# Kernel optimization log

Measured on AMD Instinct MI355X. Metric: run time of the kernel, lower is better.

Reference implementation:

```python
import jax, jax.numpy as jnp
import numpy as np


def _gcs_conv(x, a, w1, w2, b):
    # GCSConv: relu(A @ x W1 + x W2 + b);  x:[B,N,F], a:[B,N,N]
    return jax.nn.relu(jnp.einsum('bij,bjh->bih', a, x @ w1) + x @ w2 + b)


def _topk_pool(x, a, p, ratio=0.5):
    # score y = x . p/||p||, keep top ceil(ratio*N) nodes per graph,
    # gate kept node features with sigmoid(y), slice adjacency rows+cols.
    y = x @ (p / jnp.linalg.norm(p))            # [B, N]
    k = int(np.ceil(ratio * y.shape[1]))
    yk, idx = jax.lax.top_k(y, k)               # [B, k]
    xk = jnp.take_along_axis(x, idx[:, :, None], axis=1)
    xk = xk * jax.nn.sigmoid(yk)[:, :, None]    # gated node features [B,k,H]
    ak = jnp.take_along_axis(a, idx[:, :, None], axis=1)
    ak = jnp.take_along_axis(ak, idx[:, None, :], axis=2)  # [B,k,k]
    return xk, ak


def setup_inputs() -> dict:
    B, N, F0, H, C = 256, 512, 128, 32, 16
    key = jax.random.key(0)
    ks = jax.random.split(key, 12)
    s = lambda fan: 1.0 / np.sqrt(fan)
    return {
        'x': jax.random.normal(ks[0], (B, N, F0), jnp.float32),
        'a': jax.random.uniform(ks[1], (B, N, N), jnp.float32),
        'w1_1': jax.random.normal(ks[2], (F0, H), jnp.float32) * s(F0),
        'w2_1': jax.random.normal(ks[3], (F0, H), jnp.float32) * s(F0),
        'b1': jnp.zeros((H,), jnp.float32),
        'w1_2': jax.random.normal(ks[4], (H, H), jnp.float32) * s(H),
        'w2_2': jax.random.normal(ks[5], (H, H), jnp.float32) * s(H),
        'b2': jnp.zeros((H,), jnp.float32),
        'w1_3': jax.random.normal(ks[6], (H, H), jnp.float32) * s(H),
        'w2_3': jax.random.normal(ks[7], (H, H), jnp.float32) * s(H),
        'b3': jnp.zeros((H,), jnp.float32),
        'p_pool': jax.random.normal(ks[8], (H,), jnp.float32),
        'wd': jax.random.normal(ks[9], (H, C), jnp.float32) * s(H),
        'bd': jnp.zeros((C,), jnp.float32),
    }


def reference(x, a, w1_1, w2_1, b1, w1_2, w2_2, b2, w1_3, w2_3, b3, p_pool, wd, bd):
    x = _gcs_conv(x, a, w1_1, w2_1, b1)
    # NOTE: original code reuses pool1 twice -> shared p_pool for both stages
    x1, a1 = _topk_pool(x, a, p_pool)
    x1 = _gcs_conv(x1, a1, w1_2, w2_2, b2)
    x2, a2 = _topk_pool(x1, a1, p_pool)
    x2 = _gcs_conv(x2, a2, w1_3, w2_3, b3)
    pooled = jnp.mean(x2, axis=1)               # GlobalAvgPool over nodes [B,H]
    return jax.nn.softmax(pooled @ wd + bd, axis=-1)
```

## Files before the change

kernel.cpp:

```cpp
#include <hip/hip_runtime.h>
#include <cmath>

#define B 256
#define N0 512
#define F0 128
#define H 32
#define NC 16

typedef short v8s __attribute__((ext_vector_type(8)));
typedef float v4f __attribute__((ext_vector_type(4)));

__device__ inline ushort bf16_rne(float f) {
  unsigned u = __float_as_uint(f);
  unsigned r = (u + 0x7FFF + ((u >> 16) & 1)) >> 16;
  return (ushort)r;
}
__device__ inline float bf16_f(ushort s) { return __uint_as_float((unsigned)s << 16); }

template<int F, int RPT>
__global__ __launch_bounds__(256) void k_xw(
    const float* __restrict__ x, const float* __restrict__ w1,
    const float* __restrict__ w2, const float* __restrict__ bias,
    float* __restrict__ h, float* __restrict__ g) {
  __shared__ float w1t[H][F + 4];
  __shared__ float w2t[H][F + 4];
  __shared__ float bs[H];
  const int tid = threadIdx.x;
  for (int i = tid; i < F * H; i += 256) {
    int f = i >> 5, hc = i & 31;
    w1t[hc][f] = w1[i];
    w2t[hc][f] = w2[i];
  }
  if (tid < H) bs[tid] = bias[tid];
  __syncthreads();
  const int hq = tid & 7;
  const int rq = tid >> 3;
  const size_t row0 = (size_t)blockIdx.x * (32 * RPT) + (size_t)rq * RPT;
  const float* xb = x + row0 * F;
  float acc1[RPT][4];
  float acc2[RPT][4];
  #pragma unroll
  for (int r = 0; r < RPT; ++r)
    for (int c = 0; c < 4; ++c) { acc1[r][c] = 0.f; acc2[r][c] = 0.f; }
  for (int f0 = 0; f0 < F; f0 += 4) {
    float4 w1v[4], w2v[4];
    #pragma unroll
    for (int hh = 0; hh < 4; ++hh) {
      w1v[hh] = *(const float4*)&w1t[hq * 4 + hh][f0];
      w2v[hh] = *(const float4*)&w2t[hq * 4 + hh][f0];
    }
    #pragma unroll
    for (int r = 0; r < RPT; ++r) {
      float4 xv = *(const float4*)(xb + (size_t)r * F + f0);
      #pragma unroll
      for (int hh = 0; hh < 4; ++hh) {
        acc1[r][hh] += xv.x * w1v[hh].x + xv.y * w1v[hh].y + xv.z * w1v[hh].z + xv.w * w1v[hh].w;
        acc2[r][hh] += xv.x * w2v[hh].x + xv.y * w2v[hh].y + xv.z * w2v[hh].z + xv.w * w2v[hh].w;
      }
    }
  }
  #pragma unroll
  for (int r = 0; r < RPT; ++r) {
    size_t o = (row0 + r) * H + hq * 4;
    float4 hv = make_float4(acc1[r][0], acc1[r][1], acc1[r][2], acc1[r][3]);
    float4 gv = make_float4(acc2[r][0] + bs[hq * 4 + 0], acc2[r][1] + bs[hq * 4 + 1],
                            acc2[r][2] + bs[hq * 4 + 2], acc2[r][3] + bs[hq * 4 + 3]);
    *(float4*)(h + o) = hv;
    *(float4*)(g + o) = gv;
  }
}

__global__ __launch_bounds__(256) void k_trans_d(
    const float* __restrict__ hsrc, ushort* __restrict__ hTh, ushort* __restrict__ hTl) {
  __shared__ ushort thi[H][72];
  __shared__ ushort tlo[H][72];
  const int tid = threadIdx.x;
  const int b = blockIdx.x;
  const int jr = tid >> 2, kq = tid & 3;
  const int hh = tid >> 3, seg = tid & 7;
  for (int j0 = 0; j0 < N0; j0 += 64) {
    if (j0) __syncthreads();
    const float* src = hsrc + (((size_t)b * N0) + j0 + jr) * H + kq * 8;
    float4 v0 = *(const float4*)src;
    float4 v1 = *(const float4*)(src + 4);
    float vv[8] = {v0.x, v0.y, v0.z, v0.w, v1.x, v1.y, v1.z, v1.w};
    #pragma unroll
    for (int i = 0; i < 8; ++i) {
      ushort hi = bf16_rne(vv[i]);
      thi[kq * 8 + i][jr] = hi;
      tlo[kq * 8 + i][jr] = bf16_rne(vv[i] - bf16_f(hi));
    }
    __syncthreads();
    size_t o = ((size_t)b * H + hh) * N0 + j0 + seg * 8;
    *(uint4*)&hTh[o] = *(const uint4*)&thi[hh][seg * 8];
    *(uint4*)&hTl[o] = *(const uint4*)&tlo[hh][seg * 8];
  }
}

template<int K>
__global__ __launch_bounds__(256) void k_trans_s(
    const float* __restrict__ hd, const int* __restrict__ idx,
    ushort* __restrict__ hTh, ushort* __restrict__ hTl) {
  const int tid = threadIdx.x;
  const int b = blockIdx.x;
  for (int t = tid; t < K * 4; t += 256) {
    int row = t >> 2, kq = t & 3;
    int gid = idx[(size_t)b * K + row];
    const float* src = hd + (((size_t)b * K) + row) * H + kq * 8;
    float4 v0 = *(const float4*)src;
    float4 v1 = *(const float4*)(src + 4);
    float vv[8] = {v0.x, v0.y, v0.z, v0.w, v1.x, v1.y, v1.z, v1.w};
    #pragma unroll
    for (int i = 0; i < 8; ++i) {
      ushort hi = bf16_rne(vv[i]);
      size_t o = ((size_t)b * H + kq * 8 + i) * N0 + gid;
      hTh[o] = hi;
      hTl[o] = bf16_rne(vv[i] - bf16_f(hi));
    }
  }
}

template<int NROW>
__global__ __launch_bounds__(256) void k_ammx(
    const float* __restrict__ a0, const int* __restrict__ rid,
    const ushort* __restrict__ hTh, const ushort* __restrict__ hTl,
    const float* __restrict__ g, float* __restrict__ out) {
  constexpr int RB = 64;
  constexpr int KC = 32;
  constexpr int ASP = KC + 8;
  __shared__ ushort ah[RB][ASP];
  __shared__ ushort al[RB][ASP];
  __shared__ ushort bh[H][ASP];
  __shared__ ushort bl[H][ASP];
  __shared__ int rowid[RB];
  const int tid = threadIdx.x;
  const int b = blockIdx.x;
  const int row0 = blockIdx.y * RB;
  if (tid < RB) rowid[tid] = rid ? rid[(size_t)b * NROW + row0 + tid] : row0 + tid;
  __syncthreads();
  const int wave = tid >> 6, lane = tid & 63;
  const int m = lane & 15, quad = lane >> 4;
  const int sr = tid >> 2, skq = tid & 3;
  const int shh = tid >> 3, sseg = tid & 7;
  const float* abase = a0 + (size_t)b * N0 * N0;
  const ushort* bhsrc = hTh + ((size_t)b * H + shh) * N0 + sseg * 4;
  const ushort* blsrc = hTl + ((size_t)b * H + shh) * N0 + sseg * 4;
  v4f acc0 = {0.f, 0.f, 0.f, 0.f};
  v4f acc1 = {0.f, 0.f, 0.f, 0.f};
  for (int k0 = 0; k0 < N0; k0 += KC) {
    if (k0) __syncthreads();
    {
      const float* ap = abase + (size_t)rowid[sr] * N0 + k0 + skq * 4;
      float4 v0 = *(const float4*)ap;
      float4 v1 = *(const float4*)(ap + 16);
      ushort4 h0, l0, h1, l1;
      h0.x = bf16_rne(v0.x); l0.x = bf16_rne(v0.x - bf16_f(h0.x));
      h0.y = bf16_rne(v0.y); l0.y = bf16_rne(v0.y - bf16_f(h0.y));
      h0.z = bf16_rne(v0.z); l0.z = bf16_rne(v0.z - bf16_f(h0.z));
      h0.w = bf16_rne(v0.w); l0.w = bf16_rne(v0.w - bf16_f(h0.w));
      h1.x = bf16_rne(v1.x); l1.x = bf16_rne(v1.x - bf16_f(h1.x));
      h1.y = bf16_rne(v1.y); l1.y = bf16_rne(v1.y - bf16_f(h1.y));
      h1.z = bf16_rne(v1.z); l1.z = bf16_rne(v1.z - bf16_f(h1.z));
      h1.w = bf16_rne(v1.w); l1.w = bf16_rne(v1.w - bf16_f(h1.w));
      *(ushort4*)&ah[sr][skq * 4] = h0;      *(ushort4*)&al[sr][skq * 4] = l0;
      *(ushort4*)&ah[sr][skq * 4 + 16] = h1; *(ushort4*)&al[sr][skq * 4 + 16] = l1;
    }
    {
      *(ushort4*)&bh[shh][sseg * 4] = *(const ushort4*)(bhsrc + k0);
      *(ushort4*)&bl[shh][sseg * 4] = *(const ushort4*)(blsrc + k0);
    }
    __syncthreads();
    const int arow = wave * 16 + m;
    v8s Ah = *(const v8s*)&ah[arow][quad * 8];
    v8s Al = *(const v8s*)&al[arow][quad * 8];
    v8s Bh0 = *(const v8s*)&bh[m][quad * 8];
    v8s Bh1 = *(const v8s*)&bh[16 + m][quad * 8];
    v8s Bl0 = *(const v8s*)&bl[m][quad * 8];
    v8s Bl1 = *(const v8s*)&bl[16 + m][quad * 8];
    acc0 = __builtin_amdgcn_mfma_f32_16x16x32_bf16(Ah, Bh0, acc0, 0, 0, 0);
    acc1 = __builtin_amdgcn_mfma_f32_16x16x32_bf16(Ah, Bh1, acc1, 0, 0, 0);
    acc0 = __builtin_amdgcn_mfma_f32_16x16x32_bf16(Al, Bh0, acc0, 0, 0, 0);
    acc1 = __builtin_amdgcn_mfma_f32_16x16x32_bf16(Al, Bh1, acc1, 0, 0, 0);
    acc0 = __builtin_amdgcn_mfma_f32_16x16x32_bf16(Ah, Bl0, acc0, 0, 0, 0);
    acc1 = __builtin_amdgcn_mfma_f32_16x16x32_bf16(Ah, Bl1, acc1, 0, 0, 0);
  }
  #pragma unroll
  for (int reg = 0; reg < 4; ++reg) {
    int row = row0 + wave * 16 + quad * 4 + reg;
    size_t o0 = ((size_t)b * NROW + row) * H + m;
    size_t o1 = o0 + 16;
    float v0 = acc0[reg] + g[o0];
    float v1 = acc1[reg] + g[o1];
    out[o0] = fmaxf(v0, 0.f);
    out[o1] = fmaxf(v1, 0.f);
  }
}

__global__ __launch_bounds__(256) void k_zero(float4* __restrict__ p, int n4) {
  int i = blockIdx.x * 256 + threadIdx.x;
  if (i < n4) p[i] = make_float4(0.f, 0.f, 0.f, 0.f);
}

template<int NN, int K>
__global__ __launch_bounds__(256) void k_topk(
    const float* __restrict__ x, const float* __restrict__ p,
    const int* __restrict__ prev_idx,
    float* __restrict__ xg, int* __restrict__ out_idx) {
  __shared__ float ys[NN];
  __shared__ int is[NN];
  __shared__ float ps[H];
  __shared__ float pns;
  const int tid = threadIdx.x;
  const int b = blockIdx.x;
  if (tid < H) ps[tid] = p[tid];
  __syncthreads();
  if (tid == 0) {
    float s = 0.f;
    for (int i = 0; i < H; ++i) s += ps[i] * ps[i];
    pns = 1.f / sqrtf(s);
  }
  __syncthreads();
  for (int i = tid; i < NN; i += 256) {
    const float* xr = x + ((size_t)b * NN + i) * H;
    float s = 0.f;
    #pragma unroll
    for (int f = 0; f < H; ++f) s += xr[f] * ps[f];
    ys[i] = s * pns;
    is[i] = i;
  }
  for (int k = 2; k <= NN; k <<= 1) {
    for (int j = k >> 1; j > 0; j >>= 1) {
      __syncthreads();
      for (int i = tid; i < NN; i += 256) {
        int ixj = i ^ j;
        if (ixj > i) {
          float v0 = ys[i], v1 = ys[ixj];
          int i0 = is[i], i1 = is[ixj];
          bool pre = (v1 > v0) || (v1 == v0 && i1 < i0);
          bool doswap = ((i & k) == 0) ? pre : !pre;
          if (doswap) { ys[i] = v1; ys[ixj] = v0; is[i] = i1; is[ixj] = i0; }
        }
      }
    }
  }
  for (int k = 2; k <= K; k <<= 1) {
    for (int j = k >> 1; j > 0; j >>= 1) {
      __syncthreads();
      for (int i = tid; i < K; i += 256) {
        int ixj = i ^ j;
        if (ixj > i && ixj < K) {
          float v0 = ys[i], v1 = ys[ixj];
          int i0 = is[i], i1 = is[ixj];
          bool pre = (i1 < i0);
          bool doswap = ((i & k) == 0) ? pre : !pre;
          if (doswap) { ys[i] = v1; ys[ixj] = v0; is[i] = i1; is[ixj] = i0; }
        }
      }
    }
  }
  __syncthreads();
  for (int t = tid; t < K * H; t += 256) {
    int kk = t >> 5, f = t & 31;
    int loc = is[kk];
    float gate = 1.f / (1.f + expf(-ys[kk]));
    xg[((size_t)b * K + kk) * H + f] = x[((size_t)b * NN + loc) * H + f] * gate;
  }
  for (int t = tid; t < K; t += 256)
    out_idx[(size_t)b * K + t] = prev_idx ? prev_idx[(size_t)b * NN + is[t]] : is[t];
}

__global__ __launch_bounds__(128) void k_head(
    const float* __restrict__ xl3, const float* __restrict__ wd,
    const float* __restrict__ bd, float* __restrict__ out) {
  __shared__ float part[4][H];
  __shared__ float pooled[H];
  __shared__ float wds[H * NC];
  __shared__ float logits[NC];
  const int tid = threadIdx.x;
  const int b = blockIdx.x;
  for (int i = tid; i < H * NC; i += 128) wds[i] = wd[i];
  const int f = tid & 31, nq = tid >> 5;
  float s = 0.f;
  for (int n = nq * 32; n < nq * 32 + 32; ++n)
    s += xl3[((size_t)b * 128 + n) * H + f];
  part[nq][f] = s;
  __syncthreads();
  if (tid < H)
    pooled[tid] = (part[0][tid] + part[1][tid] + part[2][tid] + part[3][tid]) * (1.f / 128.f);
  __syncthreads();
  if (tid < NC) {
    float acc = bd[tid];
    for (int i = 0; i < H; ++i) acc += pooled[i] * wds[i * NC + tid];
    logits[tid] = acc;
  }
  __syncthreads();
  if (tid == 0) {
    float mx = logits[0];
    for (int i = 1; i < NC; ++i) mx = fmaxf(mx, logits[i]);
    float e[NC], se = 0.f;
    for (int i = 0; i < NC; ++i) { e[i] = expf(logits[i] - mx); se += e[i]; }
    float inv = 1.f / se;
    for (int i = 0; i < NC; ++i) out[(size_t)b * NC + i] = e[i] * inv;
  }
}

extern "C" void kernel_launch(void* const* d_in, const int* in_sizes, int n_in,
                              void* d_out, int out_size, void* d_ws, size_t ws_size,
                              hipStream_t stream) {
  (void)in_sizes; (void)n_in; (void)out_size; (void)ws_size;
  const float* x    = (const float*)d_in[0];
  const float* a    = (const float*)d_in[1];
  const float* w1_1 = (const float*)d_in[2];
  const float* w2_1 = (const float*)d_in[3];
  const float* b1   = (const float*)d_in[4];
  const float* w1_2 = (const float*)d_in[5];
  const float* w2_2 = (const float*)d_in[6];
  const float* b2   = (const float*)d_in[7];
  const float* w1_3 = (const float*)d_in[8];
  const float* w2_3 = (const float*)d_in[9];
  const float* b3   = (const float*)d_in[10];
  const float* pp   = (const float*)d_in[11];
  const float* wd   = (const float*)d_in[12];
  const float* bd   = (const float*)d_in[13];
  float* out = (float*)d_out;

  char* w = (char*)d_ws;
  auto take = [&](size_t bytes) { char* r = w; w += (bytes + 255) & ~(size_t)255; return r; };
  float*  h1  = (float*) take((size_t)B * N0 * H * 4);
  float*  g1  = (float*) take((size_t)B * N0 * H * 4);
  ushort* hTh = (ushort*)take((size_t)B * H * N0 * 2);
  ushort* hTl = (ushort*)take((size_t)B * H * N0 * 2);
  float*  xl1 = (float*) take((size_t)B * N0 * H * 4);
  int*    id1 = (int*)   take((size_t)B * 256 * 4);
  float*  xg1 = (float*) take((size_t)B * 256 * H * 4);
  float*  h2  = (float*) take((size_t)B * 256 * H * 4);
  float*  g2  = (float*) take((size_t)B * 256 * H * 4);
  float*  xl2 = (float*) take((size_t)B * 256 * H * 4);
  int*    id2 = (int*)   take((size_t)B * 128 * 4);
  float*  xg2 = (float*) take((size_t)B * 128 * H * 4);
  float*  h3  = (float*) take((size_t)B * 128 * H * 4);
  float*  g3  = (float*) take((size_t)B * 128 * H * 4);
  float*  xl3 = (float*) take((size_t)B * 128 * H * 4);
  const int hT4 = (int)((size_t)B * H * N0 * 2 * 2 / 16);

  k_xw<F0, 2><<<dim3(B * N0 / 64), dim3(256), 0, stream>>>(x, w1_1, w2_1, b1, h1, g1);
  k_trans_d<<<dim3(B), dim3(256), 0, stream>>>(h1, hTh, hTl);
  k_ammx<512><<<dim3(B, 8), dim3(256), 0, stream>>>(a, nullptr, hTh, hTl, g1, xl1);
  k_topk<512, 256><<<dim3(B), dim3(256), 0, stream>>>(xl1, pp, nullptr, xg1, id1);
  k_xw<H, 4><<<dim3(B * 256 / 128), dim3(256), 0, stream>>>(xg1, w1_2, w2_2, b2, h2, g2);
  k_zero<<<dim3((hT4 + 255) / 256), dim3(256), 0, stream>>>((float4*)hTh, hT4);
  k_trans_s<256><<<dim3(B), dim3(256), 0, stream>>>(h2, id1, hTh, hTl);
  k_ammx<256><<<dim3(B, 4), dim3(256), 0, stream>>>(a, id1, hTh, hTl, g2, xl2);
  k_topk<256, 128><<<dim3(B), dim3(256), 0, stream>>>(xl2, pp, id1, xg2, id2);
  k_xw<H, 4><<<dim3(B * 128 / 128), dim3(256), 0, stream>>>(xg2, w1_3, w2_3, b3, h3, g3);
  k_zero<<<dim3((hT4 + 255) / 256), dim3(256), 0, stream>>>((float4*)hTh, hT4);
  k_trans_s<128><<<dim3(B), dim3(256), 0, stream>>>(h3, id2, hTh, hTl);
  k_ammx<128><<<dim3(B, 2), dim3(256), 0, stream>>>(a, id2, hTh, hTl, g3, xl3);
  k_head<<<dim3(B), dim3(128), 0, stream>>>(xl3, wd, bd, out);
}
```

Before: 601.6 us.

## Fuse transposes, pooling scores, and gated gathers into neighboring GCS kernels

The first XW kernel now writes the bf16 hi/lo transposed H directly, which removes the separate transpose pass and the fp32 h1 round trip. The A·H kernel computes the top-k score y in its epilogue through shuffle reductions, so top-k only sorts a precomputed score vector. The gather-and-gate step moves into the next XW kernel, using indices plus per-row gates, which relies on linearity to scale the outputs. Scatter transposes become an inverse-index dense write that also removes the separate zeroing kernels. The catch is the extra epilogue work in the A·H kernel and irregular gathered loads in XW.

```diff
diff --git a/kernel.cpp b/kernel.cpp
--- a/kernel.cpp
+++ b/kernel.cpp
@@ -9,6 +9,7 @@
 
 typedef short v8s __attribute__((ext_vector_type(8)));
 typedef float v4f __attribute__((ext_vector_type(4)));
+typedef unsigned short v8u __attribute__((ext_vector_type(8)));
 
 __device__ inline ushort bf16_rne(float f) {
   unsigned u = __float_as_uint(f);
@@ -18,13 +19,15 @@
 __device__ inline float bf16_f(ushort s) { return __uint_as_float((unsigned)s << 16); }
 
 template<int F, int RPT>
-__global__ __launch_bounds__(256) void k_xw(
+__global__ __launch_bounds__(256) void k_xw1(
     const float* __restrict__ x, const float* __restrict__ w1,
     const float* __restrict__ w2, const float* __restrict__ bias,
-    float* __restrict__ h, float* __restrict__ g) {
+    ushort* __restrict__ hTh, ushort* __restrict__ hTl, float* __restrict__ g) {
   __shared__ float w1t[H][F + 4];
   __shared__ float w2t[H][F + 4];
   __shared__ float bs[H];
+  __shared__ __align__(16) ushort thi[H][72];
+  __shared__ __align__(16) ushort tlo[H][72];
   const int tid = threadIdx.x;
   for (int i = tid; i < F * H; i += 256) {
     int f = i >> 5, hc = i & 31;
@@ -62,61 +65,121 @@
   #pragma unroll
   for (int r = 0; r < RPT; ++r) {
     size_t o = (row0 + r) * H + hq * 4;
-    float4 hv = make_float4(acc1[r][0], acc1[r][1], acc1[r][2], acc1[r][3]);
-    float4 gv = make_float4(acc2[r][0] + bs[hq * 4 + 0], acc2[r][1] + bs[hq * 4 + 1],
-                            acc2[r][2] + bs[hq * 4 + 2], acc2[r][3] + bs[hq * 4 + 3]);
-    *(float4*)(h + o) = hv;
-    *(float4*)(g + o) = gv;
-  }
-}
-
-__global__ __launch_bounds__(256) void k_trans_d(
-    const float* __restrict__ hsrc, ushort* __restrict__ hTh, ushort* __restrict__ hTl) {
-  __shared__ ushort thi[H][72];
-  __shared__ ushort tlo[H][72];
-  const int tid = threadIdx.x;
-  const int b = blockIdx.x;
-  const int jr = tid >> 2, kq = tid & 3;
-  const int hh = tid >> 3, seg = tid & 7;
-  for (int j0 = 0; j0 < N0; j0 += 64) {
-    if (j0) __syncthreads();
-    const float* src = hsrc + (((size_t)b * N0) + j0 + jr) * H + kq * 8;
-    float4 v0 = *(const float4*)src;
-    float4 v1 = *(const float4*)(src + 4);
-    float vv[8] = {v0.x, v0.y, v0.z, v0.w, v1.x, v1.y, v1.z, v1.w};
-    #pragma unroll
-    for (int i = 0; i < 8; ++i) {
-      ushort hi = bf16_rne(vv[i]);
-      thi[kq * 8 + i][jr] = hi;
-      tlo[kq * 8 + i][jr] = bf16_rne(vv[i] - bf16_f(hi));
-    }
-    __syncthreads();
-    size_t o = ((size_t)b * H + hh) * N0 + j0 + seg * 8;
-    *(uint4*)&hTh[o] = *(const uint4*)&thi[hh][seg * 8];
-    *(uint4*)&hTl[o] = *(const uint4*)&tlo[hh][seg * 8];
+    *(float4*)(g + o) = make_float4(acc2[r][0] + bs[hq * 4 + 0], acc2[r][1] + bs[hq * 4 + 1],
+                                    acc2[r][2] + bs[hq * 4 + 2], acc2[r][3] + bs[hq * 4 + 3]);
+    #pragma unroll
+    for (int c = 0; c < 4; ++c) {
+      float v = acc1[r][c];
+      ushort hi = bf16_rne(v);
+      thi[hq * 4 + c][rq * RPT + r] = hi;
+      tlo[hq * 4 + c][rq * RPT + r] = bf16_rne(v - bf16_f(hi));
+    }
+  }
+  __syncthreads();
+  const int b = blockIdx.x >> 3;
+  const int j0 = (blockIdx.x & 7) * 64;
+  const int hrow = tid >> 3, seg = tid & 7;
+  size_t o = ((size_t)b * H + hrow) * N0 + j0 + seg * 8;
+  *(uint4*)&hTh[o] = *(const uint4*)&thi[hrow][seg * 8];
+  *(uint4*)&hTl[o] = *(const uint4*)&tlo[hrow][seg * 8];
+}
+
+template<int NPREV, int K, int RPT>
+__global__ __launch_bounds__(256) void k_xwg(
+    const float* __restrict__ xsrc, const int* __restrict__ lidx,
+    const float* __restrict__ gate,
+    const float* __restrict__ w1, const float* __restrict__ w2,
+    const float* __restrict__ bias,
+    float* __restrict__ h, float* __restrict__ g) {
+  constexpr int F = H;
+  __shared__ float w1t[H][F + 4];
+  __shared__ float w2t[H][F + 4];
+  __shared__ float bs[H];
+  const int tid = threadIdx.x;
+  for (int i = tid; i < F * H; i += 256) {
+    int f = i >> 5, hc = i & 31;
+    w1t[hc][f] = w1[i];
+    w2t[hc][f] = w2[i];
+  }
+  if (tid < H) bs[tid] = bias[tid];
+  __syncthreads();
+  const int hq = tid & 7;
+  const int rq = tid >> 3;
+  const int row0 = blockIdx.x * (32 * RPT) + rq * RPT;
+  const int b = row0 / K;
+  const float* xg0 = xsrc + (size_t)b * NPREV * H;
+  int li[RPT];
+  float gt[RPT];
+  #pragma unroll
+  for (int r = 0; r < RPT; ++r) { li[r] = lidx[row0 + r]; gt[r] = gate[row0 + r]; }
+  float acc1[RPT][4];
+  float acc2[RPT][4];
+  #pragma unroll
+  for (int r = 0; r < RPT; ++r)
+    for (int c = 0; c < 4; ++c) { acc1[r][c] = 0.f; acc2[r][c] = 0.f; }
+  for (int f0 = 0; f0 < F; f0 += 4) {
+    float4 w1v[4], w2v[4];
+    #pragma unroll
+    for (int hh = 0; hh < 4; ++hh) {
+      w1v[hh] = *(const float4*)&w1t[hq * 4 + hh][f0];
+      w2v[hh] = *(const float4*)&w2t[hq * 4 + hh][f0];
+    }
+    #pragma unroll
+    for (int r = 0; r < RPT; ++r) {
+      float4 xv = *(const float4*)(xg0 + (size_t)li[r] * H + f0);
+      #pragma unroll
+      for (int hh = 0; hh < 4; ++hh) {
+        acc1[r][hh] += xv.x * w1v[hh].x + xv.y * w1v[hh].y + xv.z * w1v[hh].z + xv.w * w1v[hh].w;
+        acc2[r][hh] += xv.x * w2v[hh].x + xv.y * w2v[hh].y + xv.z * w2v[hh].z + xv.w * w2v[hh].w;
+      }
+    }
+  }
+  #pragma unroll
+  for (int r = 0; r < RPT; ++r) {
+    size_t o = ((size_t)row0 + r) * H + hq * 4;
+    *(float4*)(h + o) = make_float4(acc1[r][0] * gt[r], acc1[r][1] * gt[r],
+                                    acc1[r][2] * gt[r], acc1[r][3] * gt[r]);
+    *(float4*)(g + o) = make_float4(acc2[r][0] * gt[r] + bs[hq * 4 + 0],
+                                    acc2[r][1] * gt[r] + bs[hq * 4 + 1],
+                                    acc2[r][2] * gt[r] + bs[hq * 4 + 2],
+                                    acc2[r][3] * gt[r] + bs[hq * 4 + 3]);
   }
 }
 
 template<int K>
-__global__ __launch_bounds__(256) void k_trans_s(
+__global__ __launch_bounds__(512) void k_trans_inv(
     const float* __restrict__ hd, const int* __restrict__ idx,
     ushort* __restrict__ hTh, ushort* __restrict__ hTl) {
+  __shared__ float hs[K][33];
+  __shared__ int inv[N0];
   const int tid = threadIdx.x;
   const int b = blockIdx.x;
-  for (int t = tid; t < K * 4; t += 256) {
-    int row = t >> 2, kq = t & 3;
-    int gid = idx[(size_t)b * K + row];
-    const float* src = hd + (((size_t)b * K) + row) * H + kq * 8;
-    float4 v0 = *(const float4*)src;
-    float4 v1 = *(const float4*)(src + 4);
-    float vv[8] = {v0.x, v0.y, v0.z, v0.w, v1.x, v1.y, v1.z, v1.w};
+  for (int j = tid; j < N0; j += 512) inv[j] = -1;
+  __syncthreads();
+  for (int k = tid; k < K; k += 512) inv[idx[(size_t)b * K + k]] = k;
+  for (int t = tid; t < K * 8; t += 512) {
+    int r = t >> 3, c4 = t & 7;
+    float4 v = *(const float4*)(hd + (((size_t)b * K) + r) * H + c4 * 4);
+    hs[r][c4 * 4 + 0] = v.x;
+    hs[r][c4 * 4 + 1] = v.y;
+    hs[r][c4 * 4 + 2] = v.z;
+    hs[r][c4 * 4 + 3] = v.w;
+  }
+  __syncthreads();
+  for (int t = tid; t < H * 64; t += 512) {
+    int hr = t >> 6, seg = t & 63;
+    v8u hv, lv;
     #pragma unroll
     for (int i = 0; i < 8; ++i) {
-      ushort hi = bf16_rne(vv[i]);
-      size_t o = ((size_t)b * H + kq * 8 + i) * N0 + gid;
-      hTh[o] = hi;
-      hTl[o] = bf16_rne(vv[i] - bf16_f(hi));
-    }
+      int k = inv[seg * 8 + i];
+      float v = (k >= 0) ? hs[k][hr] : 0.f;
+      ushort hi = bf16_rne(v);
+      hv[i] = hi;
+      lv[i] = bf16_rne(v - bf16_f(hi));
+    }
+    size_t o = ((size_t)b * H + hr) * N0 + seg * 8;
+    *(v8u*)&hTh[o] = hv;
+    *(v8u*)&hTl[o] = lv;
   }
 }
 
@@ -124,7 +187,8 @@
 __global__ __launch_bounds__(256) void k_ammx(
     const float* __restrict__ a0, const int* __restrict__ rid,
     const ushort* __restrict__ hTh, const ushort* __restrict__ hTl,
-    const float* __restrict__ g, float* __restrict__ out) {
+    const float* __restrict__ g, const float* __restrict__ p,
+    float* __restrict__ out, float* __restrict__ yout) {
   constexpr int RB = 64;
   constexpr int KC = 32;
   constexpr int ASP = KC + 8;
@@ -133,11 +197,19 @@
   __shared__ ushort bh[H][ASP];
   __shared__ ushort bl[H][ASP];
   __shared__ int rowid[RB];
+  __shared__ float psu[H];
+  __shared__ float pns_s;
   const int tid = threadIdx.x;
   const int b = blockIdx.x;
   const int row0 = blockIdx.y * RB;
   if (tid < RB) rowid[tid] = rid ? rid[(size_t)b * NROW + row0 + tid] : row0 + tid;
-  __syncthreads();
+  if (yout && tid == 0) {
+    float s = 0.f;
+    for (int i = 0; i < H; ++i) s += p[i] * p[i];
+    pns_s = 1.f / sqrtf(s);
+  }
+  __syncthreads();
+  if (yout && tid < H) psu[tid] = p[tid] * pns_s;
   const int wave = tid >> 6, lane = tid & 63;
   const int m = lane & 15, quad = lane >> 4;
   const int sr = tid >> 2, skq = tid & 3;
@@ -184,48 +256,39 @@
     acc0 = __builtin_amdgcn_mfma_f32_16x16x32_bf16(Ah, Bl0, acc0, 0, 0, 0);
     acc1 = __builtin_amdgcn_mfma_f32_16x16x32_bf16(Ah, Bl1, acc1, 0, 0, 0);
   }
+  float part[4];
   #pragma unroll
   for (int reg = 0; reg < 4; ++reg) {
     int row = row0 + wave * 16 + quad * 4 + reg;
     size_t o0 = ((size_t)b * NROW + row) * H + m;
     size_t o1 = o0 + 16;
-    float v0 = acc0[reg] + g[o0];
-    float v1 = acc1[reg] + g[o1];
-    out[o0] = fmaxf(v0, 0.f);
-    out[o1] = fmaxf(v1, 0.f);
-  }
-}
-
-__global__ __launch_bounds__(256) void k_zero(float4* __restrict__ p, int n4) {
-  int i = blockIdx.x * 256 + threadIdx.x;
-  if (i < n4) p[i] = make_float4(0.f, 0.f, 0.f, 0.f);
+    float v0 = fmaxf(acc0[reg] + g[o0], 0.f);
+    float v1 = fmaxf(acc1[reg] + g[o1], 0.f);
+    out[o0] = v0;
+    out[o1] = v1;
+    if (yout) part[reg] = v0 * psu[m] + v1 * psu[m + 16];
+  }
+  if (yout) {
+    #pragma unroll
+    for (int reg = 0; reg < 4; ++reg)
+      #pragma unroll
+      for (int off = 1; off < 16; off <<= 1)
+        part[reg] += __shfl_xor(part[reg], off, 16);
+    if (m < 4)
+      yout[(size_t)b * NROW + row0 + wave * 16 + quad * 4 + m] = part[m];
+  }
 }
 
 template<int NN, int K>
 __global__ __launch_bounds__(256) void k_topk(
-    const float* __restrict__ x, const float* __restrict__ p,
-    const int* __restrict__ prev_idx,
-    float* __restrict__ xg, int* __restrict__ out_idx) {
+    const float* __restrict__ y, const int* __restrict__ prev_idx,
+    int* __restrict__ lidx, float* __restrict__ gate, int* __restrict__ out_idx) {
   __shared__ float ys[NN];
   __shared__ int is[NN];
-  __shared__ float ps[H];
-  __shared__ float pns;
   const int tid = threadIdx.x;
   const int b = blockIdx.x;
-  if (tid < H) ps[tid] = p[tid];
-  __syncthreads();
-  if (tid == 0) {
-    float s = 0.f;
-    for (int i = 0; i < H; ++i) s += ps[i] * ps[i];
-    pns = 1.f / sqrtf(s);
-  }
-  __syncthreads();
   for (int i = tid; i < NN; i += 256) {
-    const float* xr = x + ((size_t)b * NN + i) * H;
-    float s = 0.f;
-    #pragma unroll
-    for (int f = 0; f < H; ++f) s += xr[f] * ps[f];
-    ys[i] = s * pns;
+    ys[i] = y[(size_t)b * NN + i];
     is[i] = i;
   }
   for (int k = 2; k <= NN; k <<= 1) {
@@ -259,14 +322,11 @@
     }
   }
   __syncthreads();
-  for (int t = tid; t < K * H; t += 256) {
-    int kk = t >> 5, f = t & 31;
-    int loc = is[kk];
-    float gate = 1.f / (1.f + expf(-ys[kk]));
-    xg[((size_t)b * K + kk) * H + f] = x[((size_t)b * NN + loc) * H + f] * gate;
-  }
-  for (int t = tid; t < K; t += 256)
+  for (int t = tid; t < K; t += 256) {
+    lidx[(size_t)b * K + t] = is[t];
+    gate[(size_t)b * K + t] = 1.f / (1.f + expf(-ys[t]));
     out_idx[(size_t)b * K + t] = prev_idx ? prev_idx[(size_t)b * NN + is[t]] : is[t];
+  }
 }
 
 __global__ __launch_bounds__(128) void k_head(
@@ -326,35 +386,34 @@
 
   char* w = (char*)d_ws;
   auto take = [&](size_t bytes) { char* r = w; w += (bytes + 255) & ~(size_t)255; return r; };
-  float*  h1  = (float*) take((size_t)B * N0 * H * 4);
-  float*  g1  = (float*) take((size_t)B * N0 * H * 4);
   ushort* hTh = (ushort*)take((size_t)B * H * N0 * 2);
   ushort* hTl = (ushort*)take((size_t)B * H * N0 * 2);
+  float*  g1  = (float*) take((size_t)B * N0 * H * 4);
   float*  xl1 = (float*) take((size_t)B * N0 * H * 4);
+  float*  y1  = (float*) take((size_t)B * N0 * 4);
   int*    id1 = (int*)   take((size_t)B * 256 * 4);
-  float*  xg1 = (float*) take((size_t)B * 256 * H * 4);
+  int*    li1 = (int*)   take((size_t)B * 256 * 4);
+  float*  gt1 = (float*) take((size_t)B * 256 * 4);
   float*  h2  = (float*) take((size_t)B * 256 * H * 4);
   float*  g2  = (float*) take((size_t)B * 256 * H * 4);
   float*  xl2 = (float*) take((size_t)B * 256 * H * 4);
+  float*  y2  = (float*) take((size_t)B * 256 * 4);
   int*    id2 = (int*)   take((size_t)B * 128 * 4);
-  float*  xg2 = (float*) take((size_t)B * 128 * H * 4);
+  int*    li2 = (int*)   take((size_t)B * 128 * 4);
+  float*  gt2 = (float*) take((size_t)B * 128 * 4);
   float*  h3  = (float*) take((size_t)B * 128 * H * 4);
   float*  g3  = (float*) take((size_t)B * 128 * H * 4);
   float*  xl3 = (float*) take((size_t)B * 128 * H * 4);
-  const int hT4 = (int)((size_t)B * H * N0 * 2 * 2 / 16);
-
-  k_xw<F0, 2><<<dim3(B * N0 / 64), dim3(256), 0, stream>>>(x, w1_1, w2_1, b1, h1, g1);
-  k_trans_d<<<dim3(B), dim3(256), 0, stream>>>(h1, hTh, hTl);
-  k_ammx<512><<<dim3(B, 8), dim3(256), 0, stream>>>(a, nullptr, hTh, hTl, g1, xl1);
-  k_topk<512, 256><<<dim3(B), dim3(256), 0, stream>>>(xl1, pp, nullptr, xg1, id1);
-  k_xw<H, 4><<<dim3(B * 256 / 128), dim3(256), 0, stream>>>(xg1, w1_2, w2_2, b2, h2, g2);
-  k_zero<<<dim3((hT4 + 255) / 256), dim3(256), 0, stream>>>((float4*)hTh, hT4);
-  k_trans_s<256><<<dim3(B), dim3(256), 0, stream>>>(h2, id1, hTh, hTl);
-  k_ammx<256><<<dim3(B, 4), dim3(256), 0, stream>>>(a, id1, hTh, hTl, g2, xl2);
-  k_topk<256, 128><<<dim3(B), dim3(256), 0, stream>>>(xl2, pp, id1, xg2, id2);
-  k_xw<H, 4><<<dim3(B * 128 / 128), dim3(256), 0, stream>>>(xg2, w1_3, w2_3, b3, h3, g3);
-  k_zero<<<dim3((hT4 + 255) / 256), dim3(256), 0, stream>>>((float4*)hTh, hT4);
-  k_trans_s<128><<<dim3(B), dim3(256), 0, stream>>>(h3, id2, hTh, hTl);
-  k_ammx<128><<<dim3(B, 2), dim3(256), 0, stream>>>(a, id2, hTh, hTl, g3, xl3);
+
+  k_xw1<F0, 2><<<dim3(B * N0 / 64), dim3(256), 0, stream>>>(x, w1_1, w2_1, b1, hTh, hTl, g1);
+  k_ammx<512><<<dim3(B, 8), dim3(256), 0, stream>>>(a, nullptr, hTh, hTl, g1, pp, xl1, y1);
+  k_topk<512, 256><<<dim3(B), dim3(256), 0, stream>>>(y1, nullptr, li1, gt1, id1);
+  k_xwg<512, 256, 4><<<dim3(B * 256 / 128), dim3(256), 0, stream>>>(xl1, li1, gt1, w1_2, w2_2, b2, h2, g2);
+  k_trans_inv<256><<<dim3(B), dim3(512), 0, stream>>>(h2, id1, hTh, hTl);
+  k_ammx<256><<<dim3(B, 4), dim3(256), 0, stream>>>(a, id1, hTh, hTl, g2, pp, xl2, y2);
+  k_topk<256, 128><<<dim3(B), dim3(256), 0, stream>>>(y2, id1, li2, gt2, id2);
+  k_xwg<256, 128, 4><<<dim3(B * 128 / 128), dim3(256), 0, stream>>>(xl2, li2, gt2, w1_3, w2_3, b3, h3, g3);
+  k_trans_inv<128><<<dim3(B), dim3(512), 0, stream>>>(h3, id2, hTh, hTl);
+  k_ammx<128><<<dim3(B, 2), dim3(256), 0, stream>>>(a, id2, hTh, hTl, g3, nullptr, xl3, nullptr);
   k_head<<<dim3(B), dim3(128), 0, stream>>>(xl3, wd, bd, out);
 }
```

After: 585.4 us. 2.7% less time.
